# Kernel tuning notes

Hardware: AMD Instinct MI355X
Metric: run time of the kernel (lower is better)

Reference implementation:

```python
import jax, jax.numpy as jnp
import numpy as np

DIM = 96
HEADS = 8  # num_heads_v
EPS = 1e-12  # torch F.normalize eps


def conv1x1(x, w, b):
    # x: [B,C,H,W], w: [O,C,1,1], b: [O]
    y = jnp.einsum('bchw,oc->bohw', x, w[:, :, 0, 0])
    return y + b[None, :, None, None]


def dwconv3x3(x, w, b):
    # depthwise 3x3, groups == channels; w: [C,1,3,3]
    y = jax.lax.conv_general_dilated(
        x, w, window_strides=(1, 1), padding=((1, 1), (1, 1)),
        dimension_numbers=('NCHW', 'OIHW', 'NCHW'),
        feature_group_count=x.shape[1])
    return y + b[None, :, None, None]


def setup_inputs() -> dict:
    key = jax.random.key(0)
    ks = jax.random.split(key, 7)
    c = DIM
    s = 0.05
    x = jax.random.normal(ks[0], (4, c, 256, 256), jnp.float32)
    qkv_w = jax.random.normal(ks[1], (3 * c, c, 1, 1), jnp.float32) * s
    qkv_b = jax.random.normal(ks[2], (3 * c,), jnp.float32) * s
    dw_w = jax.random.normal(ks[3], (3 * c, 1, 3, 3), jnp.float32) * s
    dw_b = jax.random.normal(ks[4], (3 * c,), jnp.float32) * s
    proj_w = jax.random.normal(ks[5], (c, c, 1, 1), jnp.float32) * s
    proj_b = jax.random.normal(ks[6], (c,), jnp.float32) * s
    temperature = jnp.ones((HEADS, 1, 1), jnp.float32)
    return {"x": x, "qkv_w": qkv_w, "qkv_b": qkv_b, "dw_w": dw_w,
            "dw_b": dw_b, "proj_w": proj_w, "proj_b": proj_b,
            "temperature": temperature}


def reference(x, qkv_w, qkv_b, dw_w, dw_b, proj_w, proj_b, temperature):
    b, c, h, w = x.shape
    head = temperature.shape[0]
    w2 = w // head
    qkv = dwconv3x3(conv1x1(x, qkv_w, qkv_b), dw_w, dw_b)
    q0, k0, v0 = jnp.split(qkv, 3, axis=1)  # each [b,c,h,w]

    def to_heads(t):
        # 'b c h (head w2) -> b head w2 (c h)'
        t = t.reshape(b, c, h, head, w2)
        return jnp.transpose(t, (0, 3, 4, 1, 2)).reshape(b, head, w2, c * h)

    q = to_heads(q0)
    k = to_heads(k0)
    v = to_heads(v0)
    q = q / jnp.maximum(jnp.linalg.norm(q, axis=-1, keepdims=True), EPS)
    k = k / jnp.maximum(jnp.linalg.norm(k, axis=-1, keepdims=True), EPS)
    attn = jnp.einsum('bhid,bhjd->bhij', q, k) * temperature[None]  # [b,head,w2,w2]
    attn = jax.nn.softmax(attn, axis=-1)
    out = jnp.einsum('bhij,bhjd->bhid', attn, v)  # [b,head,w2,c*h]
    # 'b head w2 (c h) -> b c h (head w2)'
    out = out.reshape(b, head, w2, c, h)
    out = jnp.transpose(out, (0, 3, 4, 1, 2)).reshape(b, c, h, w)
    return conv1x1(out, proj_w, proj_b)
```

## Files before the change

### kernel.cpp

```cpp
#include <hip/hip_runtime.h>

#define CC 96
#define C3 288
#define HH 256
#define WW 256
#define HWC 65536
#define NHEADS 8
#define W2 32

typedef __bf16 bf16x8 __attribute__((ext_vector_type(8)));
typedef float f32x4 __attribute__((ext_vector_type(4)));
typedef unsigned short us8v __attribute__((ext_vector_type(8)));

__device__ __forceinline__ float bf2f(unsigned short u) {
  return __uint_as_float(((unsigned)u) << 16);
}
__device__ __forceinline__ unsigned short f2bf(float f) {
  unsigned u = __float_as_uint(f);
  unsigned r = u + 0x7fffu + ((u >> 16) & 1u);
  return (unsigned short)(r >> 16);
}

__global__ __launch_bounds__(256, 4) void k1_qkv_mfma(
    const float* __restrict__ x, const float* __restrict__ qw,
    const float* __restrict__ qb, unsigned short* __restrict__ pre, int b0)
{
  __shared__ __align__(16) unsigned short As2[2][64 * 106];
  const int t = threadIdx.x;
  const int o0 = blockIdx.y * 96;
  const int bz = blockIdx.z;
  const float* xb = x + (size_t)(b0 + bz) * CC * HWC;

  const int wave = t >> 6, lane = t & 63;
  const int wm = wave & 1, wn = wave >> 1;
  const int row = lane & 15, kg = lane >> 4;

  bf16x8 bfr[3][3];
  float bias[3];
#pragma unroll
  for (int nt = 0; nt < 3; ++nt) {
    int ocl = wn * 48 + nt * 16 + row;
    bias[nt] = qb[o0 + ocl];
#pragma unroll
    for (int kk = 0; kk < 3; ++kk) {
      const float* wp = qw + (size_t)(o0 + ocl) * 96 + kk * 32 + kg * 8;
      float4 w0 = *reinterpret_cast<const float4*>(wp);
      float4 w1 = *reinterpret_cast<const float4*>(wp + 4);
      us8v u;
      u[0] = f2bf(w0.x); u[1] = f2bf(w0.y); u[2] = f2bf(w0.z); u[3] = f2bf(w0.w);
      u[4] = f2bf(w1.x); u[5] = f2bf(w1.y); u[6] = f2bf(w1.z); u[7] = f2bf(w1.w);
      bfr[kk][nt] = *reinterpret_cast<bf16x8*>(&u);
    }
  }

  int sic[3], sp4[3];
#pragma unroll
  for (int r = 0; r < 3; ++r) {
    int lin = r * 256 + t;
    sic[r] = lin >> 4;
    sp4[r] = (lin & 15) * 4;
  }

  int p0 = blockIdx.x * 512;
  float4 va0[3], va1[3];
#pragma unroll
  for (int r = 0; r < 3; ++r) {
    va0[r] = *reinterpret_cast<const float4*>(xb + (size_t)(2 * sic[r]) * HWC + p0 + sp4[r]);
    va1[r] = *reinterpret_cast<const float4*>(xb + (size_t)(2 * sic[r] + 1) * HWC + p0 + sp4[r]);
  }

  for (int i = 0; i < 8; ++i) {
    unsigned short* Ac = As2[i & 1];
#pragma unroll
    for (int r = 0; r < 3; ++r) {
      float a0[4] = {va0[r].x, va0[r].y, va0[r].z, va0[r].w};
      float a1[4] = {va1[r].x, va1[r].y, va1[r].z, va1[r].w};
#pragma unroll
      for (int j = 0; j < 4; ++j) {
        unsigned pk = (unsigned)f2bf(a0[j]) | ((unsigned)f2bf(a1[j]) << 16);
        *reinterpret_cast<unsigned*>(&Ac[(sp4[r] + j) * 106 + 2 * sic[r]]) = pk;
      }
    }
    if (i < 7) {
      int p0n = p0 + 64;
#pragma unroll
      for (int r = 0; r < 3; ++r) {
        va0[r] = *reinterpret_cast<const float4*>(xb + (size_t)(2 * sic[r]) * HWC + p0n + sp4[r]);
        va1[r] = *reinterpret_cast<const float4*>(xb + (size_t)(2 * sic[r] + 1) * HWC + p0n + sp4[r]);
      }
    }
    __syncthreads();

    f32x4 acc[2][3];
#pragma unroll
    for (int mt = 0; mt < 2; ++mt)
#pragma unroll
      for (int nt = 0; nt < 3; ++nt) acc[mt][nt] = (f32x4){0.f, 0.f, 0.f, 0.f};
#pragma unroll
    for (int kk = 0; kk < 3; ++kk) {
      bf16x8 a[2];
#pragma unroll
      for (int mt = 0; mt < 2; ++mt)
        a[mt] = *reinterpret_cast<const bf16x8*>(
            &Ac[(wm * 32 + mt * 16 + row) * 106 + kk * 32 + kg * 8]);
#pragma unroll
      for (int mt = 0; mt < 2; ++mt)
#pragma unroll
        for (int nt = 0; nt < 3; ++nt)
          acc[mt][nt] = __builtin_amdgcn_mfma_f32_16x16x32_bf16(
              a[mt], bfr[kk][nt], acc[mt][nt], 0, 0, 0);
    }
    __syncthreads();

    unsigned short* tD = (unsigned short*)As2;
#pragma unroll
    for (int nt = 0; nt < 3; ++nt) {
      int ocl = wn * 48 + nt * 16 + row;
      float bv = bias[nt];
#pragma unroll
      for (int mt = 0; mt < 2; ++mt) {
        int pxl = wm * 32 + mt * 16 + kg * 4;
        f32x4 v = acc[mt][nt];
        unsigned pk0 = (unsigned)f2bf(v[0] + bv) | ((unsigned)f2bf(v[1] + bv) << 16);
        unsigned pk1 = (unsigned)f2bf(v[2] + bv) | ((unsigned)f2bf(v[3] + bv) << 16);
        *reinterpret_cast<unsigned*>(&tD[ocl * 72 + pxl]) = pk0;
        *reinterpret_cast<unsigned*>(&tD[ocl * 72 + pxl + 2]) = pk1;
      }
    }
    __syncthreads();
    unsigned short* preb = pre + ((size_t)bz * C3 + o0) * HWC + p0;
#pragma unroll
    for (int r = 0; r < 3; ++r) {
      int lin = r * 256 + t;
      int oc = lin >> 3, ch = lin & 7;
      us8v v = *reinterpret_cast<const us8v*>(&tD[oc * 72 + ch * 8]);
      *reinterpret_cast<us8v*>(preb + (size_t)oc * HWC + ch * 8) = v;
    }
    __syncthreads();
    p0 += 64;
  }
}

__global__ __launch_bounds__(256, 4) void k3_gram(
    const unsigned short* __restrict__ pre, const float* __restrict__ dww,
    const float* __restrict__ dwb, float* __restrict__ gpart,
    float* __restrict__ ssq)
{
  __shared__ __align__(16) unsigned short qT[32 * 264];
  __shared__ __align__(16) unsigned short kT[32 * 264];
  const int t = threadIdx.x;
  const int cg0 = blockIdx.x;
  const int head = blockIdx.y, bz = blockIdx.z;
  const int lane = t & 63, wave = t >> 6;
  const int mt = wave & 1, nt = wave >> 1;
  const int l15 = lane & 15, l4 = lane >> 4;
  const int hgroup = t >> 2;
  const int lw = t & 3;
  const int h0 = hgroup * 4;
  const int w0 = head * W2 + lw * 8;

  f32x4 acc = (f32x4){0.f, 0.f, 0.f, 0.f};
  float ssum_q = 0.f, ssum_k = 0.f;
  float o[4][8];

  for (int cc = 0; cc < 4; ++cc) {
    const int cq = cg0 * 4 + cc;
#pragma unroll
    for (int tensor = 0; tensor < 2; ++tensor) {
      const int ch = (tensor ? CC : 0) + cq;
      const unsigned short* src = pre + ((size_t)bz * C3 + ch) * HWC;
      const float* wg9 = dww + ch * 9;
      const float bias = dwb[ch];

      us8v rin[6];
#pragma unroll
      for (int r = 0; r < 6; ++r) {
        int hh = h0 - 1 + r;
        rin[r] = (hh >= 0 && hh < HH)
            ? *reinterpret_cast<const us8v*>(src + (size_t)hh * WW + w0)
            : (us8v){0, 0, 0, 0, 0, 0, 0, 0};
      }
      float eL[6], eR[6];
#pragma unroll
      for (int r = 0; r < 6; ++r) { eL[r] = 0.f; eR[r] = 0.f; }
      if (lw == 0 && head > 0) {
#pragma unroll
        for (int r = 0; r < 6; ++r) {
          int hh = h0 - 1 + r;
          if (hh >= 0 && hh < HH) eL[r] = bf2f(src[(size_t)hh * WW + w0 - 1]);
        }
      }
      if (lw == 3 && head < 7) {
#pragma unroll
        for (int r = 0; r < 6; ++r) {
          int hh = h0 - 1 + r;
          if (hh >= 0 && hh < HH) eR[r] = bf2f(src[(size_t)hh * WW + w0 + 8]);
        }
      }
      float f[6][8], lf[6], rt[6];
#pragma unroll
      for (int r = 0; r < 6; ++r) {
#pragma unroll
        for (int j = 0; j < 8; ++j) f[r][j] = bf2f(rin[r][j]);
        float l = __shfl_up(f[r][7], 1);
        float rr = __shfl_down(f[r][0], 1);
        lf[r] = (lw == 0) ? eL[r] : l;
        rt[r] = (lw == 3) ? eR[r] : rr;
      }
#pragma unroll
      for (int orow = 0; orow < 4; ++orow) {
#pragma unroll
        for (int j = 0; j < 8; ++j) o[orow][j] = bias;
#pragma unroll
        for (int k = 0; k < 3; ++k) {
          const int r = orow + k;
          const float w0_ = wg9[k * 3 + 0], w1_ = wg9[k * 3 + 1], w2_ = wg9[k * 3 + 2];
          o[orow][0] = fmaf(lf[r], w0_, fmaf(f[r][0], w1_, fmaf(f[r][1], w2_, o[orow][0])));
#pragma unroll
          for (int j = 1; j < 7; ++j)
            o[orow][j] = fmaf(f[r][j - 1], w0_, fmaf(f[r][j], w1_, fmaf(f[r][j + 1], w2_, o[orow][j])));
          o[orow][7] = fmaf(f[r][6], w0_, fmaf(f[r][7], w1_, fmaf(rt[r], w2_, o[orow][7])));
        }
      }
      if (tensor == 0) {
        __syncthreads();
        unsigned* dst = reinterpret_cast<unsigned*>(qT);
#pragma unroll
        for (int j = 0; j < 8; ++j)
#pragma unroll
          for (int p = 0; p < 2; ++p)
            dst[(lw * 8 + j) * 132 + hgroup * 2 + p] =
                (unsigned)f2bf(o[2 * p][j]) | ((unsigned)f2bf(o[2 * p + 1][j]) << 16);
#pragma unroll
        for (int orow = 0; orow < 4; ++orow)
#pragma unroll
          for (int j = 0; j < 8; ++j) ssum_q = fmaf(o[orow][j], o[orow][j], ssum_q);
      } else {
        unsigned* dst = reinterpret_cast<unsigned*>(kT);
#pragma unroll
        for (int j = 0; j < 8; ++j)
#pragma unroll
          for (int p = 0; p < 2; ++p)
            dst[(lw * 8 + j) * 132 + hgroup * 2 + p] =
                (unsigned)f2bf(o[2 * p][j]) | ((unsigned)f2bf(o[2 * p + 1][j]) << 16);
#pragma unroll
        for (int orow = 0; orow < 4; ++orow)
#pragma unroll
          for (int j = 0; j < 8; ++j) ssum_k = fmaf(o[orow][j], o[orow][j], ssum_k);
      }
    }
    __syncthreads();
#pragma unroll
    for (int kk = 0; kk < 8; ++kk) {
      bf16x8 a = *reinterpret_cast<const bf16x8*>(
          &qT[(mt * 16 + l15) * 264 + kk * 32 + l4 * 8]);
      bf16x8 b = *reinterpret_cast<const bf16x8*>(
          &kT[(nt * 16 + l15) * 264 + kk * 32 + l4 * 8]);
      acc = __builtin_amdgcn_mfma_f32_16x16x32_bf16(a, b, acc, 0, 0, 0);
    }
  }

  float* gp = gpart + (((size_t)bz * NHEADS + head) * 24 + cg0) * 1024;
#pragma unroll
  for (int reg = 0; reg < 4; ++reg)
    gp[(nt * 16 + l15) * 32 + mt * 16 + l4 * 4 + reg] = acc[reg];

  __syncthreads();
  float* red = reinterpret_cast<float*>(qT);
  red[t] = ssum_q;
  red[256 + t] = ssum_k;
  __syncthreads();
  if (t < 32) {
    float sq = 0.f, sk = 0.f;
#pragma unroll
    for (int p = 0; p < 8; ++p) { sq += red[t + 32 * p]; sk += red[256 + t + 32 * p]; }
    atomicAdd(&ssq[(size_t)bz * 512 + head * W2 + t], sq);
    atomicAdd(&ssq[(size_t)bz * 512 + 256 + head * W2 + t], sk);
  }
}

__global__ __launch_bounds__(256) void k4b_softmax(
    const float* __restrict__ gpart, const float* __restrict__ ssq,
    const float* __restrict__ temp, float* __restrict__ attn)
{
  __shared__ float lg[1024];
  const int t = threadIdx.x;
  const int head = blockIdx.x, bz = blockIdx.y;
  const float* gp = gpart + ((size_t)bz * NHEADS + head) * 24 * 1024;
  float4 s = make_float4(0.f, 0.f, 0.f, 0.f);
#pragma unroll 4
  for (int cg = 0; cg < 24; ++cg) {
    float4 v = *reinterpret_cast<const float4*>(gp + cg * 1024 + t * 4);
    s.x += v.x; s.y += v.y; s.z += v.z; s.w += v.w;
  }
  *reinterpret_cast<float4*>(&lg[t * 4]) = s;
  __syncthreads();
  if (t < 32) {
    const int i = t;
    const float* sq_ = ssq + (size_t)bz * 512 + head * W2;
    const float* sk_ = ssq + (size_t)bz * 512 + 256 + head * W2;
    float invq = 1.f / fmaxf(sqrtf(sq_[i]), 1e-12f);
    float tpq = temp[head] * invq;
    float rowv[32];
    float m = -1e30f;
#pragma unroll
    for (int j = 0; j < 32; ++j) {
      float invk = 1.f / fmaxf(sqrtf(sk_[j]), 1e-12f);
      float v = lg[j * 32 + i] * tpq * invk;
      rowv[j] = v;
      m = fmaxf(m, v);
    }
    float ssum = 0;
#pragma unroll
    for (int j = 0; j < 32; ++j) { rowv[j] = expf(rowv[j] - m); ssum += rowv[j]; }
    float inv = 1.f / ssum;
    float* ap = attn + ((size_t)bz * NHEADS + head) * 1024 + i * 32;
#pragma unroll
    for (int j = 0; j < 32; ++j) ap[j] = rowv[j] * inv;
  }
}

__global__ __launch_bounds__(256) void k5a_attnv(
    const unsigned short* __restrict__ pre, const float* __restrict__ dww,
    const float* __restrict__ dwb, const float* __restrict__ attn,
    unsigned short* __restrict__ tbuf)
{
  __shared__ __align__(16) unsigned short vsm[64 * 264];
  __shared__ __align__(16) unsigned short atn_s[256 * 36];
  const int t = threadIdx.x;
  const int tile = blockIdx.x;
  const int bz = blockIdx.y;
  const size_t R0 = (size_t)tile * 64;
  const int c = tile >> 2;
  const int h0 = (tile & 3) * 64;
  const unsigned short* vsrc = pre + ((size_t)bz * C3 + 2 * CC + c) * HWC;
  const int team = t >> 5, tl = t & 31;

  float4 av[8];
  {
    const float* ap = attn + (size_t)bz * 8192 + t * 32;
#pragma unroll
    for (int k = 0; k < 8; ++k)
      av[k] = *reinterpret_cast<const float4*>(ap + k * 4);
  }

  float wg[9];
#pragma unroll
  for (int i = 0; i < 9; ++i) wg[i] = dww[(2 * CC + c) * 9 + i];
  const float vbias = dwb[2 * CC + c];

#pragma unroll
  for (int p = 0; p < 2; ++p) {
    const int hb = h0 + team * 8 + p * 4;
    us8v rin[6];
#pragma unroll
    for (int r = 0; r < 6; ++r) {
      int hh = hb - 1 + r;
      if (hh >= 0 && hh < HH)
        rin[r] = *reinterpret_cast<const us8v*>(vsrc + (size_t)hh * WW + tl * 8);
      else
        rin[r] = (us8v){0, 0, 0, 0, 0, 0, 0, 0};
    }
    float f[6][8], lf[6], rt[6];
#pragma unroll
    for (int r = 0; r < 6; ++r) {
#pragma unroll
      for (int j = 0; j < 8; ++j) f[r][j] = bf2f(rin[r][j]);
      float l = __shfl_up(f[r][7], 1, 32);
      float rr = __shfl_down(f[r][0], 1, 32);
      lf[r] = (tl == 0) ? 0.f : l;
      rt[r] = (tl == 31) ? 0.f : rr;
    }
#pragma unroll
    for (int orow = 0; orow < 4; ++orow) {
      float o[8];
#pragma unroll
      for (int j = 0; j < 8; ++j) o[j] = vbias;
#pragma unroll
      for (int k = 0; k < 3; ++k) {
        const int r = orow + k;
        const float w0 = wg[k * 3 + 0], w1 = wg[k * 3 + 1], w2 = wg[k * 3 + 2];
        o[0] = fmaf(lf[r], w0, fmaf(f[r][0], w1, fmaf(f[r][1], w2, o[0])));
#pragma unroll
        for (int j = 1; j < 7; ++j)
          o[j] = fmaf(f[r][j - 1], w0, fmaf(f[r][j], w1, fmaf(f[r][j + 1], w2, o[j])));
        o[7] = fmaf(f[r][6], w0, fmaf(f[r][7], w1, fmaf(rt[r], w2, o[7])));
      }
      us8v u;
#pragma unroll
      for (int j = 0; j < 8; ++j) u[j] = f2bf(o[j]);
      int rl = team * 8 + p * 4 + orow;
      *reinterpret_cast<us8v*>(&vsm[rl * 264 + tl * 8]) = u;
    }
  }
#pragma unroll
  for (int k = 0; k < 8; ++k) {
    ushort4 u;
    u.x = f2bf(av[k].x); u.y = f2bf(av[k].y); u.z = f2bf(av[k].z); u.w = f2bf(av[k].w);
    *reinterpret_cast<ushort4*>(&atn_s[t * 36 + k * 4]) = u;
  }
  __syncthreads();

  const int wave = t >> 6, lane = t & 63;
  const int mrow = lane & 15, kg = lane >> 4;

  bf16x8 a[8], b[16];
#pragma unroll
  for (int hd = 0; hd < 8; ++hd)
    a[hd] = *reinterpret_cast<const bf16x8*>(
        &vsm[(wave * 16 + mrow) * 264 + hd * 32 + kg * 8]);
#pragma unroll
  for (int hd = 0; hd < 8; ++hd)
#pragma unroll
    for (int it = 0; it < 2; ++it)
      b[hd * 2 + it] = *reinterpret_cast<const bf16x8*>(
          &atn_s[(hd * 32 + it * 16 + mrow) * 36 + kg * 8]);

  f32x4 acc[16];
#pragma unroll
  for (int q = 0; q < 16; ++q) acc[q] = (f32x4){0.f, 0.f, 0.f, 0.f};
#pragma unroll
  for (int hd = 0; hd < 8; ++hd)
#pragma unroll
    for (int it = 0; it < 2; ++it)
      acc[hd * 2 + it] = __builtin_amdgcn_mfma_f32_16x16x32_bf16(
          a[hd], b[hd * 2 + it], acc[hd * 2 + it], 0, 0, 0);
  __syncthreads();

#pragma unroll
  for (int hd = 0; hd < 8; ++hd)
#pragma unroll
    for (int it = 0; it < 2; ++it) {
      f32x4 v = acc[hd * 2 + it];
      int col = hd * 32 + it * 16 + mrow;
#pragma unroll
      for (int r = 0; r < 4; ++r)
        vsm[(wave * 16 + kg * 4 + r) * 264 + col] = f2bf(v[r]);
    }
  unsigned short* tdst = tbuf + (size_t)bz * CC * HWC + R0 * 256;
#pragma unroll
  for (int k = 0; k < 8; ++k) {
    int n = k * 64 + lane;
    int rloc = n >> 5, c8 = n & 31;
    us8v v = *reinterpret_cast<const us8v*>(&vsm[(wave * 16 + rloc) * 264 + c8 * 8]);
    *reinterpret_cast<us8v*>(tdst + ((size_t)(wave * 16 + rloc)) * 256 + c8 * 8) = v;
  }
}

__global__ __launch_bounds__(256, 4) void k5b_proj(
    const unsigned short* __restrict__ tbuf, const float* __restrict__ pw,
    const float* __restrict__ pb, float* __restrict__ out, int b0)
{
  __shared__ __align__(16) unsigned short As2[2][64 * 106];
  const int t = threadIdx.x;
  const int bz = blockIdx.y;
  const unsigned short* tb = tbuf + (size_t)bz * CC * HWC;

  const int wave = t >> 6, lane = t & 63;
  const int wm = wave & 1, wn = wave >> 1;
  const int row = lane & 15, kg = lane >> 4;

  bf16x8 bfr[3][3];
  float bias[3];
#pragma unroll
  for (int nt = 0; nt < 3; ++nt) {
    int ocl = wn * 48 + nt * 16 + row;
    bias[nt] = pb[ocl];
#pragma unroll
    for (int kk = 0; kk < 3; ++kk) {
      const float* wp = pw + (size_t)ocl * 96 + kk * 32 + kg * 8;
      float4 w0 = *reinterpret_cast<const float4*>(wp);
      float4 w1 = *reinterpret_cast<const float4*>(wp + 4);
      us8v u;
      u[0] = f2bf(w0.x); u[1] = f2bf(w0.y); u[2] = f2bf(w0.z); u[3] = f2bf(w0.w);
      u[4] = f2bf(w1.x); u[5] = f2bf(w1.y); u[6] = f2bf(w1.z); u[7] = f2bf(w1.w);
      bfr[kk][nt] = *reinterpret_cast<bf16x8*>(&u);
    }
  }

  int sic[3], sp4[3];
#pragma unroll
  for (int r = 0; r < 3; ++r) {
    int lin = r * 256 + t;
    sic[r] = lin >> 4;
    sp4[r] = (lin & 15) * 4;
  }

  int p0 = blockIdx.x * 512;
  ushort4 ua0[3], ua1[3];
#pragma unroll
  for (int r = 0; r < 3; ++r) {
    ua0[r] = *reinterpret_cast<const ushort4*>(tb + (size_t)(2 * sic[r]) * HWC + p0 + sp4[r]);
    ua1[r] = *reinterpret_cast<const ushort4*>(tb + (size_t)(2 * sic[r] + 1) * HWC + p0 + sp4[r]);
  }

  for (int i = 0; i < 8; ++i) {
    unsigned short* Ac = As2[i & 1];
#pragma unroll
    for (int r = 0; r < 3; ++r) {
      unsigned short a0[4] = {ua0[r].x, ua0[r].y, ua0[r].z, ua0[r].w};
      unsigned short a1[4] = {ua1[r].x, ua1[r].y, ua1[r].z, ua1[r].w};
#pragma unroll
      for (int j = 0; j < 4; ++j) {
        unsigned pk = (unsigned)a0[j] | ((unsigned)a1[j] << 16);
        *reinterpret_cast<unsigned*>(&Ac[(sp4[r] + j) * 106 + 2 * sic[r]]) = pk;
      }
    }
    if (i < 7) {
      int p0n = p0 + 64;
#pragma unroll
      for (int r = 0; r < 3; ++r) {
        ua0[r] = *reinterpret_cast<const ushort4*>(tb + (size_t)(2 * sic[r]) * HWC + p0n + sp4[r]);
        ua1[r] = *reinterpret_cast<const ushort4*>(tb + (size_t)(2 * sic[r] + 1) * HWC + p0n + sp4[r]);
      }
    }
    __syncthreads();

    f32x4 acc[2][3];
#pragma unroll
    for (int mt = 0; mt < 2; ++mt)
#pragma unroll
      for (int nt = 0; nt < 3; ++nt) acc[mt][nt] = (f32x4){0.f, 0.f, 0.f, 0.f};
#pragma unroll
    for (int kk = 0; kk < 3; ++kk) {
      bf16x8 a[2];
#pragma unroll
      for (int mt = 0; mt < 2; ++mt)
        a[mt] = *reinterpret_cast<const bf16x8*>(
            &Ac[(wm * 32 + mt * 16 + row) * 106 + kk * 32 + kg * 8]);
#pragma unroll
      for (int mt = 0; mt < 2; ++mt)
#pragma unroll
        for (int nt = 0; nt < 3; ++nt)
          acc[mt][nt] = __builtin_amdgcn_mfma_f32_16x16x32_bf16(
              a[mt], bfr[kk][nt], acc[mt][nt], 0, 0, 0);
    }
    __syncthreads();

    float* tD = (float*)As2;
#pragma unroll
    for (int nt = 0; nt < 3; ++nt) {
      int ocl = wn * 48 + nt * 16 + row;
      float bv = bias[nt];
#pragma unroll
      for (int mt = 0; mt < 2; ++mt) {
        int pxl = wm * 32 + mt * 16 + kg * 4;
        f32x4 v = acc[mt][nt];
        float4 w = make_float4(v[0] + bv, v[1] + bv, v[2] + bv, v[3] + bv);
        *reinterpret_cast<float4*>(&tD[ocl * 68 + pxl]) = w;
      }
    }
    __syncthreads();
    float* ob = out + (size_t)(b0 + bz) * CC * HWC + p0;
#pragma unroll
    for (int r = 0; r < 6; ++r) {
      int lin = r * 256 + t;
      int o = lin >> 4, p4 = (lin & 15) * 4;
      float4 v = *reinterpret_cast<const float4*>(&tD[o * 68 + p4]);
      *reinterpret_cast<float4*>(ob + (size_t)o * HWC + p4) = v;
    }
    __syncthreads();
    p0 += 64;
  }
}

extern "C" void kernel_launch(void* const* d_in, const int* in_sizes, int n_in,
                              void* d_out, int out_size, void* d_ws, size_t ws_size,
                              hipStream_t stream)
{
  const float* x      = (const float*)d_in[0];
  const float* qkv_w  = (const float*)d_in[1];
  const float* qkv_b  = (const float*)d_in[2];
  const float* dw_w   = (const float*)d_in[3];
  const float* dw_b   = (const float*)d_in[4];
  const float* proj_w = (const float*)d_in[5];
  const float* proj_b = (const float*)d_in[6];
  const float* temp   = (const float*)d_in[7];
  float* out = (float*)d_out;

  const size_t per_pre   = (size_t)C3 * HWC * 2;
  const size_t per_tbuf  = (size_t)CC * HWC * 2;
  const size_t per_ssq   = (size_t)2 * 256 * 4;
  const size_t per_attn  = (size_t)NHEADS * 1024 * 4;
  const size_t per_gpart = (size_t)NHEADS * 24 * 1024 * 4;
  const size_t per_b = per_pre + per_tbuf + per_ssq + per_attn + per_gpart;

  int bc = 4;
  while (bc > 1 && per_b * (size_t)bc > ws_size) bc >>= 1;

  char* p = (char*)d_ws;
  unsigned short* pre  = (unsigned short*)p; p += per_pre * bc;
  unsigned short* tbuf = (unsigned short*)p; p += per_tbuf * bc;
  float* ssq   = (float*)p; p += per_ssq * bc;
  float* attn  = (float*)p; p += per_attn * bc;
  float* gpart = (float*)p; p += per_gpart * bc;

  for (int b0 = 0; b0 < 4; b0 += bc) {
    k1_qkv_mfma<<<dim3(128, 3, bc), 256, 0, stream>>>(x, qkv_w, qkv_b, pre, b0);
    hipMemsetAsync(ssq, 0, per_ssq * bc, stream);
    k3_gram<<<dim3(24, NHEADS, bc), 256, 0, stream>>>(pre, dw_w, dw_b, gpart, ssq);
    k4b_softmax<<<dim3(NHEADS, bc), 256, 0, stream>>>(gpart, ssq, temp, attn);
    k5a_attnv<<<dim3(384, bc), 256, 0, stream>>>(pre, dw_w, dw_b, attn, tbuf);
    k5b_proj<<<dim3(128, bc), 256, 0, stream>>>(tbuf, proj_w, proj_b, out, b0);
  }
}
```

Baseline: 222.9 us.

## Make QKV 1x1-conv kernel wave-private to drop block barriers

The QKV projection kernel is restructured so each wave owns a private LDS tile of 32 pixels and computes all 96 output channels for it, instead of the block sharing a 64-pixel tile split across waves. This removes every __syncthreads from the loop, since waves only touch their own LDS region. Each wave now stages its own bias-added bf16 output in two halves of 48 channels. The cost is twice as many weight fragments and accumulators per thread, and launch bounds are lowered to 3 blocks per CU to make room. The register prefetch of the next input tile is gone, so global-load latency is no longer hidden inside a block.

```diff
diff --git a/kernel.cpp b/kernel.cpp
--- a/kernel.cpp
+++ b/kernel.cpp
@@ -21,25 +21,25 @@
   return (unsigned short)(r >> 16);
 }
 
-__global__ __launch_bounds__(256, 4) void k1_qkv_mfma(
+__global__ __launch_bounds__(256, 3) void k1_qkv_mfma(
     const float* __restrict__ x, const float* __restrict__ qw,
     const float* __restrict__ qb, unsigned short* __restrict__ pre, int b0)
 {
-  __shared__ __align__(16) unsigned short As2[2][64 * 106];
+  __shared__ __align__(16) unsigned short As4[4][32 * 106];
   const int t = threadIdx.x;
   const int o0 = blockIdx.y * 96;
   const int bz = blockIdx.z;
   const float* xb = x + (size_t)(b0 + bz) * CC * HWC;
 
   const int wave = t >> 6, lane = t & 63;
-  const int wm = wave & 1, wn = wave >> 1;
   const int row = lane & 15, kg = lane >> 4;
-
-  bf16x8 bfr[3][3];
-  float bias[3];
-#pragma unroll
-  for (int nt = 0; nt < 3; ++nt) {
-    int ocl = wn * 48 + nt * 16 + row;
+  unsigned short* Aw = &As4[wave][0];
+
+  bf16x8 bfr[3][6];
+  float bias[6];
+#pragma unroll
+  for (int nt = 0; nt < 6; ++nt) {
+    int ocl = nt * 16 + row;
     bias[nt] = qb[o0 + ocl];
 #pragma unroll
     for (int kk = 0; kk < 3; ++kk) {
@@ -53,91 +53,73 @@
     }
   }
 
-  int sic[3], sp4[3];
-#pragma unroll
-  for (int r = 0; r < 3; ++r) {
-    int lin = r * 256 + t;
-    sic[r] = lin >> 4;
-    sp4[r] = (lin & 15) * 4;
-  }
-
-  int p0 = blockIdx.x * 512;
-  float4 va0[3], va1[3];
-#pragma unroll
-  for (int r = 0; r < 3; ++r) {
-    va0[r] = *reinterpret_cast<const float4*>(xb + (size_t)(2 * sic[r]) * HWC + p0 + sp4[r]);
-    va1[r] = *reinterpret_cast<const float4*>(xb + (size_t)(2 * sic[r] + 1) * HWC + p0 + sp4[r]);
-  }
-
-  for (int i = 0; i < 8; ++i) {
-    unsigned short* Ac = As2[i & 1];
-#pragma unroll
-    for (int r = 0; r < 3; ++r) {
-      float a0[4] = {va0[r].x, va0[r].y, va0[r].z, va0[r].w};
-      float a1[4] = {va1[r].x, va1[r].y, va1[r].z, va1[r].w};
+  const int icp0 = lane >> 3;
+  const int px4 = (lane & 7) * 4;
+
+  for (int iter = 0; iter < 4; ++iter) {
+    const int p0 = blockIdx.x * 512 + iter * 128 + wave * 32;
+
+#pragma unroll
+    for (int r = 0; r < 6; ++r) {
+      int icp = r * 8 + icp0;
+      float4 v0 = *reinterpret_cast<const float4*>(xb + (size_t)(2 * icp) * HWC + p0 + px4);
+      float4 v1 = *reinterpret_cast<const float4*>(xb + (size_t)(2 * icp + 1) * HWC + p0 + px4);
+      float a0[4] = {v0.x, v0.y, v0.z, v0.w};
+      float a1[4] = {v1.x, v1.y, v1.z, v1.w};
 #pragma unroll
       for (int j = 0; j < 4; ++j) {
         unsigned pk = (unsigned)f2bf(a0[j]) | ((unsigned)f2bf(a1[j]) << 16);
-        *reinterpret_cast<unsigned*>(&Ac[(sp4[r] + j) * 106 + 2 * sic[r]]) = pk;
-      }
-    }
-    if (i < 7) {
-      int p0n = p0 + 64;
-#pragma unroll
-      for (int r = 0; r < 3; ++r) {
-        va0[r] = *reinterpret_cast<const float4*>(xb + (size_t)(2 * sic[r]) * HWC + p0n + sp4[r]);
-        va1[r] = *reinterpret_cast<const float4*>(xb + (size_t)(2 * sic[r] + 1) * HWC + p0n + sp4[r]);
-      }
-    }
-    __syncthreads();
-
-    f32x4 acc[2][3];
+        *reinterpret_cast<unsigned*>(&Aw[(px4 + j) * 106 + 2 * icp]) = pk;
+      }
+    }
+
+    f32x4 acc[2][6];
 #pragma unroll
     for (int mt = 0; mt < 2; ++mt)
 #pragma unroll
-      for (int nt = 0; nt < 3; ++nt) acc[mt][nt] = (f32x4){0.f, 0.f, 0.f, 0.f};
+      for (int nt = 0; nt < 6; ++nt) acc[mt][nt] = (f32x4){0.f, 0.f, 0.f, 0.f};
 #pragma unroll
     for (int kk = 0; kk < 3; ++kk) {
       bf16x8 a[2];
 #pragma unroll
       for (int mt = 0; mt < 2; ++mt)
         a[mt] = *reinterpret_cast<const bf16x8*>(
-            &Ac[(wm * 32 + mt * 16 + row) * 106 + kk * 32 + kg * 8]);
+            &Aw[(mt * 16 + row) * 106 + kk * 32 + kg * 8]);
 #pragma unroll
       for (int mt = 0; mt < 2; ++mt)
 #pragma unroll
-        for (int nt = 0; nt < 3; ++nt)
+        for (int nt = 0; nt < 6; ++nt)
           acc[mt][nt] = __builtin_amdgcn_mfma_f32_16x16x32_bf16(
               a[mt], bfr[kk][nt], acc[mt][nt], 0, 0, 0);
     }
-    __syncthreads();
-
-    unsigned short* tD = (unsigned short*)As2;
-#pragma unroll
-    for (int nt = 0; nt < 3; ++nt) {
-      int ocl = wn * 48 + nt * 16 + row;
-      float bv = bias[nt];
-#pragma unroll
-      for (int mt = 0; mt < 2; ++mt) {
-        int pxl = wm * 32 + mt * 16 + kg * 4;
-        f32x4 v = acc[mt][nt];
-        unsigned pk0 = (unsigned)f2bf(v[0] + bv) | ((unsigned)f2bf(v[1] + bv) << 16);
-        unsigned pk1 = (unsigned)f2bf(v[2] + bv) | ((unsigned)f2bf(v[3] + bv) << 16);
-        *reinterpret_cast<unsigned*>(&tD[ocl * 72 + pxl]) = pk0;
-        *reinterpret_cast<unsigned*>(&tD[ocl * 72 + pxl + 2]) = pk1;
-      }
-    }
-    __syncthreads();
-    unsigned short* preb = pre + ((size_t)bz * C3 + o0) * HWC + p0;
-#pragma unroll
-    for (int r = 0; r < 3; ++r) {
-      int lin = r * 256 + t;
-      int oc = lin >> 3, ch = lin & 7;
-      us8v v = *reinterpret_cast<const us8v*>(&tD[oc * 72 + ch * 8]);
-      *reinterpret_cast<us8v*>(preb + (size_t)oc * HWC + ch * 8) = v;
-    }
-    __syncthreads();
-    p0 += 64;
+
+    unsigned short* tD = Aw;
+#pragma unroll
+    for (int half = 0; half < 2; ++half) {
+#pragma unroll
+      for (int nt3 = 0; nt3 < 3; ++nt3) {
+        int nt = half * 3 + nt3;
+        int ocL = nt3 * 16 + row;
+        float bv = bias[nt];
+#pragma unroll
+        for (int mt = 0; mt < 2; ++mt) {
+          int pxl = mt * 16 + kg * 4;
+          f32x4 v = acc[mt][nt];
+          unsigned pk0 = (unsigned)f2bf(v[0] + bv) | ((unsigned)f2bf(v[1] + bv) << 16);
+          unsigned pk1 = (unsigned)f2bf(v[2] + bv) | ((unsigned)f2bf(v[3] + bv) << 16);
+          *reinterpret_cast<unsigned*>(&tD[ocL * 40 + pxl]) = pk0;
+          *reinterpret_cast<unsigned*>(&tD[ocL * 40 + pxl + 2]) = pk1;
+        }
+      }
+      unsigned short* preb = pre + ((size_t)bz * C3 + o0 + half * 48) * HWC + p0;
+#pragma unroll
+      for (int p = 0; p < 3; ++p) {
+        int lin = p * 64 + lane;
+        int ocL = lin >> 2, ch = lin & 3;
+        us8v v = *reinterpret_cast<const us8v*>(&tD[ocL * 40 + ch * 8]);
+        *reinterpret_cast<us8v*>(preb + (size_t)ocL * HWC + ch * 8) = v;
+      }
+    }
   }
 }
 
```

Measured after the change: 292.5 us. 31.2% more time.
